# Performance work log

Hardware: AMD Instinct MI355X
Metric: run time of the kernel (lower is better)

Reference implementation:

```python
import jax, jax.numpy as jnp
import numpy as np
from functools import partial

BETA_F = 1.0        # layer default beta_f
DOUBLING_ITERS = 21 # covers tree depth up to 2**21; random recursive tree depth ~ O(log N)


def setup_inputs() -> dict:
    key = jax.random.key(0)
    ks = jax.random.split(key, 6)
    N, K = 2_000_000, 8
    H, W = 2048, 2048
    attrs2d = jax.random.uniform(ks[0], (N, K), dtype=jnp.float32)  # normalized attrs in [a,1]
    weight = jax.random.normal(ks[1], (K,), dtype=jnp.float32)
    bias = jax.random.normal(ks[2], (1,), dtype=jnp.float32)
    levels = jax.random.uniform(ks[3], (N,), dtype=jnp.float32)
    # valid component tree: parent[i] < i for i>0, root = 0
    u = jax.random.uniform(ks[4], (N,))
    parent = jnp.floor(u * jnp.arange(N, dtype=jnp.float32)).astype(jnp.int32)
    pixel_node = jax.random.randint(ks[5], (H, W), 0, N, dtype=jnp.int32)
    return {"attrs2d": attrs2d, "weight": weight, "bias": bias,
            "levels": levels, "parent": parent, "pixel_node": pixel_node}


def _tree_filter(sigmoid, levels, parent, pixel_node):
    """Connected (direct-rule) filtering on a component tree.

    Each node contributes sigma(node) * (level(node) - level(parent));
    the filtered value of a pixel is the sum of contributions along the
    root-to-node path (root contributes its full level).
    Path sums are computed with pointer doubling (fully vectorized).
    """
    N = levels.shape[0]
    contrib = sigmoid * (levels - levels[parent])          # (N,)
    contrib = contrib.at[0].set(levels[0])                 # root keeps its level
    # sentinel node N with zero contribution, parent of root -> sentinel
    contrib_e = jnp.concatenate([contrib, jnp.zeros((1,), contrib.dtype)])
    par_e = jnp.concatenate([parent.at[0].set(N), jnp.array([N], jnp.int32)])

    def step(carry, _):
        s, p = carry
        return (s + s[p], p[p]), None

    (s, _), _ = jax.lax.scan(step, (contrib_e, par_e), None, length=DOUBLING_ITERS)
    y_nodes = s[:N]                                        # filtered gray value per node
    return y_nodes[pixel_node]                             # (H, W)


def reference(attrs2d, weight, bias, levels, parent, pixel_node):
    logits = attrs2d @ weight + bias[0]                    # (N,)
    s = BETA_F * logits                                    # clamp_logits=False (layer default)
    sigmoid = jax.nn.sigmoid(s)
    return _tree_filter(sigmoid, levels, parent, pixel_node)
```

## Files before the change

kernel.cpp:

```cpp
#include <hip/hip_runtime.h>
#include <hip/hip_fp16.h>

typedef float vf4 __attribute__((ext_vector_type(4)));
typedef int   vi4 __attribute__((ext_vector_type(4)));

struct SP { float s; int p; };

__device__ __forceinline__ SP ldSP(const SP* __restrict__ ptr) {
    float2 v = *reinterpret_cast<const float2*>(ptr);
    SP r; r.s = v.x; r.p = __float_as_int(v.y);
    return r;
}
__device__ __forceinline__ void stSP(SP* __restrict__ ptr, float s, int p) {
    float2 v; v.x = s; v.y = __int_as_float(p);
    *reinterpret_cast<float2*>(ptr) = v;
}

__global__ void k_contrib(const float* __restrict__ attrs,
                          const float* __restrict__ weight,
                          const float* __restrict__ bias,
                          const float* __restrict__ levels,
                          const int*   __restrict__ parent,
                          SP* __restrict__ buf, int N) {
    float w0 = weight[0], w1 = weight[1], w2 = weight[2], w3 = weight[3];
    float w4 = weight[4], w5 = weight[5], w6 = weight[6], w7 = weight[7];
    float b = bias[0];
    int stride = gridDim.x * blockDim.x;
    const vf4* a4 = reinterpret_cast<const vf4*>(attrs);
    for (int i = blockIdx.x * blockDim.x + threadIdx.x; i < N; i += stride) {
        vf4 a0 = __builtin_nontemporal_load(&a4[2 * (size_t)i]);
        vf4 a1 = __builtin_nontemporal_load(&a4[2 * (size_t)i + 1]);
        float x = a0.x * w0 + a0.y * w1 + a0.z * w2 + a0.w * w3
                + a1.x * w4 + a1.y * w5 + a1.z * w6 + a1.w * w7 + b;
        float sg = 1.0f / (1.0f + __expf(-x));
        int p = parent[i];
        float c = sg * (levels[i] - levels[p]);
        if (i == 0) {
            stSP(&buf[0], levels[0], N);
        } else {
            stSP(&buf[i], c, p);
        }
    }
}

__global__ void k_level(const SP* __restrict__ buf,
                        float* __restrict__ yAll,
                        __half* __restrict__ y16,
                        int lo, int hi, int N) {
    int i = lo + blockIdx.x * blockDim.x + threadIdx.x;
    if (i >= hi) return;
    float acc = 0.0f;
    int p = i;
    while (p >= lo && p < N) {
        SP w = ldSP(&buf[p]);
        acc += w.s;
        p = w.p;
    }
    if (p < lo) acc += yAll[p];
    yAll[i] = acc;
    y16[i] = __float2half(acc);
}

__global__ void k_gather(const __half* __restrict__ y,
                         const int*   __restrict__ pix,
                         float*       __restrict__ out, int M) {
    int stride = gridDim.x * blockDim.x;
    int M4 = M >> 2;
    const vi4* pix4 = reinterpret_cast<const vi4*>(pix);
    vf4* out4 = reinterpret_cast<vf4*>(out);
    for (int i = blockIdx.x * blockDim.x + threadIdx.x; i < M4; i += stride) {
        vi4 p = __builtin_nontemporal_load(&pix4[i]);
        vf4 o;
        o.x = __half2float(y[p.x]);
        o.y = __half2float(y[p.y]);
        o.z = __half2float(y[p.z]);
        o.w = __half2float(y[p.w]);
        __builtin_nontemporal_store(o, &out4[i]);
    }
    int tid = blockIdx.x * blockDim.x + threadIdx.x;
    for (int i = (M4 << 2) + tid; i < M; i += stride) {
        out[i] = __half2float(y[pix[i]]);
    }
}

extern "C" void kernel_launch(void* const* d_in, const int* in_sizes, int n_in,
                              void* d_out, int out_size, void* d_ws, size_t ws_size,
                              hipStream_t stream) {
    const float* attrs  = (const float*)d_in[0];
    const float* weight = (const float*)d_in[1];
    const float* bias   = (const float*)d_in[2];
    const float* levels = (const float*)d_in[3];
    const int*   parent = (const int*)d_in[4];
    const int*   pix    = (const int*)d_in[5];
    float* out = (float*)d_out;

    const int N = in_sizes[3];
    const int M = out_size;

    SP* buf      = (SP*)d_ws;
    __half* y16  = (__half*)(buf + N);
    float* yAll  = (float*)(y16 + N);

    const int BLK = 256;

    k_contrib<<<2048, BLK, 0, stream>>>(attrs, weight, bias, levels, parent, buf, N);

    const int T0 = 0, T1 = 32768, T2 = 131072, T3 = 524288;
    k_level<<<(T1 - T0 + BLK - 1) / BLK, BLK, 0, stream>>>(buf, yAll, y16, T0, T1, N);
    k_level<<<(T2 - T1 + BLK - 1) / BLK, BLK, 0, stream>>>(buf, yAll, y16, T1, T2, N);
    k_level<<<(T3 - T2 + BLK - 1) / BLK, BLK, 0, stream>>>(buf, yAll, y16, T2, T3, N);
    k_level<<<(N  - T3 + BLK - 1) / BLK, BLK, 0, stream>>>(buf, yAll, y16, T3, N,  N);

    k_gather<<<2048, BLK, 0, stream>>>(y16, pix, out, M);
}
```

Before: 102.1 us.

## Use fp16 levels and prefix sums, drop fp32 yAll, retune level splits

Result: faster. 95.84 us (-6.2%).

```diff
diff --git a/kernel.cpp b/kernel.cpp
--- a/kernel.cpp
+++ b/kernel.cpp
@@ -16,10 +16,28 @@
     *reinterpret_cast<float2*>(ptr) = v;
 }
 
+__global__ void k_lev16(const float* __restrict__ levels,
+                        __half* __restrict__ lev, int N) {
+    int stride = gridDim.x * blockDim.x;
+    int n4 = N >> 2;
+    const vf4* l4 = reinterpret_cast<const vf4*>(levels);
+    __half2* h2 = reinterpret_cast<__half2*>(lev);
+    for (int i = blockIdx.x * blockDim.x + threadIdx.x; i < n4; i += stride) {
+        vf4 v = __builtin_nontemporal_load(&l4[i]);
+        __half2 h0; h0.x = __float2half(v.x); h0.y = __float2half(v.y);
+        __half2 h1; h1.x = __float2half(v.z); h1.y = __float2half(v.w);
+        h2[2 * i]     = h0;
+        h2[2 * i + 1] = h1;
+    }
+    for (int i = (n4 << 2) + blockIdx.x * blockDim.x + threadIdx.x; i < N; i += stride)
+        lev[i] = __float2half(levels[i]);
+}
+
 __global__ void k_contrib(const float* __restrict__ attrs,
                           const float* __restrict__ weight,
                           const float* __restrict__ bias,
                           const float* __restrict__ levels,
+                          const __half* __restrict__ lev,
                           const int*   __restrict__ parent,
                           SP* __restrict__ buf, int N) {
     float w0 = weight[0], w1 = weight[1], w2 = weight[2], w3 = weight[3];
@@ -33,18 +51,14 @@
         float x = a0.x * w0 + a0.y * w1 + a0.z * w2 + a0.w * w3
                 + a1.x * w4 + a1.y * w5 + a1.z * w6 + a1.w * w7 + b;
         float sg = 1.0f / (1.0f + __expf(-x));
-        int p = parent[i];
-        float c = sg * (levels[i] - levels[p]);
-        if (i == 0) {
-            stSP(&buf[0], levels[0], N);
-        } else {
-            stSP(&buf[i], c, p);
-        }
+        int p = __builtin_nontemporal_load(&parent[i]);
+        float c = sg * (__half2float(lev[i]) - __half2float(lev[p]));
+        if (i == 0) stSP(&buf[0], levels[0], N);
+        else        stSP(&buf[i], c, p);
     }
 }
 
 __global__ void k_level(const SP* __restrict__ buf,
-                        float* __restrict__ yAll,
                         __half* __restrict__ y16,
                         int lo, int hi, int N) {
     int i = lo + blockIdx.x * blockDim.x + threadIdx.x;
@@ -56,8 +70,7 @@
         acc += w.s;
         p = w.p;
     }
-    if (p < lo) acc += yAll[p];
-    yAll[i] = acc;
+    if (p < lo) acc += __half2float(y16[p]);
     y16[i] = __float2half(acc);
 }
 
@@ -78,9 +91,8 @@
         __builtin_nontemporal_store(o, &out4[i]);
     }
     int tid = blockIdx.x * blockDim.x + threadIdx.x;
-    for (int i = (M4 << 2) + tid; i < M; i += stride) {
+    for (int i = (M4 << 2) + tid; i < M; i += stride)
         out[i] = __half2float(y[pix[i]]);
-    }
 }
 
 extern "C" void kernel_launch(void* const* d_in, const int* in_sizes, int n_in,
@@ -97,19 +109,21 @@
     const int N = in_sizes[3];
     const int M = out_size;
 
-    SP* buf      = (SP*)d_ws;
-    __half* y16  = (__half*)(buf + N);
-    float* yAll  = (float*)(y16 + N);
+    SP*     buf   = (SP*)d_ws;
+    __half* y16   = (__half*)(buf + N);
+    __half* lev16 = (__half*)(y16 + N);
 
     const int BLK = 256;
+    #define CDIV(a,b) (((a)+(b)-1)/(b))
 
-    k_contrib<<<2048, BLK, 0, stream>>>(attrs, weight, bias, levels, parent, buf, N);
+    k_lev16  <<<1024, BLK, 0, stream>>>(levels, lev16, N);
+    k_contrib<<<2048, BLK, 0, stream>>>(attrs, weight, bias, levels, lev16, parent, buf, N);
 
-    const int T0 = 0, T1 = 32768, T2 = 131072, T3 = 524288;
-    k_level<<<(T1 - T0 + BLK - 1) / BLK, BLK, 0, stream>>>(buf, yAll, y16, T0, T1, N);
-    k_level<<<(T2 - T1 + BLK - 1) / BLK, BLK, 0, stream>>>(buf, yAll, y16, T1, T2, N);
-    k_level<<<(T3 - T2 + BLK - 1) / BLK, BLK, 0, stream>>>(buf, yAll, y16, T2, T3, N);
-    k_level<<<(N  - T3 + BLK - 1) / BLK, BLK, 0, stream>>>(buf, yAll, y16, T3, N,  N);
+    const int T1 = 32768, T2 = 524288, T3 = 1048576;
+    k_level<<<CDIV(T1,      BLK), BLK, 0, stream>>>(buf, y16, 0,  T1, N);
+    k_level<<<CDIV(T2 - T1, BLK), BLK, 0, stream>>>(buf, y16, T1, T2, N);
+    k_level<<<CDIV(T3 - T2, BLK), BLK, 0, stream>>>(buf, y16, T2, T3, N);
+    k_level<<<CDIV(N  - T3, BLK), BLK, 0, stream>>>(buf, y16, T3, N,  N);
 
     k_gather<<<2048, BLK, 0, stream>>>(y16, pix, out, M);
 }
```
